# Kernel optimization log

Hardware: AMD Instinct MI355X
Metric: run time of the kernel (lower is better)

## Reference

```python
import jax, jax.numpy as jnp
import numpy as np

B, T, I = 8, 8192, 128
E, J, K = 16, 128, 1024


def setup_inputs() -> dict:
    key = jax.random.key(0)
    k1, k2, k3 = jax.random.split(key, 3)
    X = jax.random.normal(k1, (B, T, I), dtype=jnp.float32)
    ind = jax.random.randint(k2, (B, E, K), 0, T, dtype=jnp.int64)
    # matches torch.rand(E, I, J): uniform [0, 1)
    W = jax.random.uniform(k3, (E, I, J), dtype=jnp.float32)
    return {"X": X, "ind": ind, "W": W}


def reference(X, ind, W):
    # Dense per-expert matmul over ALL tokens: Y[b,e,t,j] = sum_i X[b,t,i] W[e,i,j]
    # (torch expand is a broadcast view; einsum broadcasts directly)
    Y = jnp.einsum('bti,eij->betj', X, W)  # [B, E, T, J]
    # Gather selected tokens per (batch, expert) along the token axis
    Yg = jnp.take_along_axis(Y, ind[..., None], axis=2)  # [B, E, K, J]
    return Yg
```

## Files before the change

### kernel.cpp

```cpp
#include <hip/hip_runtime.h>

#define B_ 8
#define T_ 8192
#define I_ 128
#define E_ 16
#define J_ 128
#define K_ 1024
#define ROWS 128

typedef unsigned short u16;
typedef unsigned int   u32;
typedef __attribute__((ext_vector_type(8))) short s8v;
typedef __attribute__((ext_vector_type(4))) float f4v;

__device__ __forceinline__ u16 f2bf(float f) {
    union { float f; u32 u; } v; v.f = f;
    const u32 u = v.u;
    return (u16)((u + 0x7fffu + ((u >> 16) & 1u)) >> 16);
}

__global__ __launch_bounds__(512, 4)
void gather_mfma(const float* __restrict__ X, const int* __restrict__ ind,
                 const float* __restrict__ W, float* __restrict__ Y) {
    __shared__ u16 WsT[I_ * J_];
    __shared__ u16 Xs[ROWS * I_];

    const int t    = threadIdx.x;
    const int wave = t >> 6;
    const int lane = t & 63;

    const int orig = blockIdx.x;
    const int bid  = (orig & 7) * 64 + (orig >> 3);
    const int kh = bid & 3;
    const int be = bid >> 2;
    const int e  = be & (E_ - 1);
    const int b  = be >> 4;
    const int k0 = kh * (2 * ROWS);

    const int ch   = lane & 31;
    const int rsub = lane >> 5;
    int idxA[8], idxB[8];
#pragma unroll
    for (int u = 0; u < 8; ++u) {
        const int rw = wave * 2 + rsub + 16 * u;
        idxA[u] = ind[(size_t)be * K_ + k0 + rw];
        idxB[u] = ind[(size_t)be * K_ + k0 + ROWS + rw];
    }

    {
        const float* We = W + (size_t)e * (I_ * J_);
        const int io = t & 15;
        const int j0 = (t >> 4) * 4;
        float4 w4[8];
#pragma unroll
        for (int u = 0; u < 8; ++u)
            w4[u] = *reinterpret_cast<const float4*>(We + (size_t)(io * 8 + u) * J_ + j0);
#pragma unroll
        for (int qq = 0; qq < 4; ++qq) {
            const int j = j0 + qq;
            s8v o;
#pragma unroll
            for (int u = 0; u < 8; ++u) {
                const float* wf = reinterpret_cast<const float*>(&w4[u]);
                o[u] = (short)f2bf(wf[qq]);
            }
            *reinterpret_cast<s8v*>((char*)WsT + ((j * 256 + io * 16) ^ ((j & 7) << 4))) = o;
        }
    }

    float4 v[8];
    auto load_rows = [&](const int* idxs) {
#pragma unroll
        for (int u = 0; u < 8; ++u)
            v[u] = reinterpret_cast<const float4*>(X + ((size_t)b * T_ + idxs[u]) * I_)[ch];
    };
    auto pack_write = [&]() {
#pragma unroll
        for (int u = 0; u < 8; ++u) {
            const int rw = wave * 2 + rsub + 16 * u;
            const float4 a = v[u];
            uint2 o;
            o.x = ((u32)f2bf(a.y) << 16) | f2bf(a.x);
            o.y = ((u32)f2bf(a.w) << 16) | f2bf(a.z);
            *reinterpret_cast<uint2*>((char*)Xs + rw * 256 + ((ch * 8) ^ ((rw & 7) << 4))) = o;
        }
    };

    load_rows(idxA);
    pack_write();
    __syncthreads();

    const int rq  = wave >> 1;
    const int jh  = wave & 1;
    const int g   = lane >> 4;
    const int l15 = lane & 15;
    const int sx  = (lane & 7) << 4;
    const char* xb = (const char*)Xs  + (size_t)(rq * 32 + l15) * 256;
    const char* wb = (const char*)WsT + (size_t)(jh * 64 + l15) * 256;

    auto compute_store = [&](int kbase) {
        s8v af[2][4];
#pragma unroll
        for (int s = 0; s < 4; ++s) {
            const int off = (s * 64 + g * 16) ^ sx;
            af[0][s] = *reinterpret_cast<const s8v*>(xb + off);
            af[1][s] = *reinterpret_cast<const s8v*>(xb + 16 * 256 + off);
        }
        float* Yb = Y + ((size_t)be * K_ + kbase) * J_;
#pragma unroll
        for (int n = 0; n < 4; ++n) {
            f4v acc0, acc1;
#pragma unroll
            for (int rr = 0; rr < 4; ++rr) { acc0[rr] = 0.f; acc1[rr] = 0.f; }
#pragma unroll
            for (int s = 0; s < 4; ++s) {
                const int off = (s * 64 + g * 16) ^ sx;
                const s8v bf = *reinterpret_cast<const s8v*>(wb + n * 16 * 256 + off);
                acc0 = __builtin_amdgcn_mfma_f32_16x16x32_bf16(af[0][s], bf, acc0, 0, 0, 0);
                acc1 = __builtin_amdgcn_mfma_f32_16x16x32_bf16(af[1][s], bf, acc1, 0, 0, 0);
            }
            const int col = jh * 64 + n * 16 + l15;
            const int row0 = rq * 32 + g * 4;
#pragma unroll
            for (int rr = 0; rr < 4; ++rr)
                Yb[(size_t)(row0 + rr) * J_ + col] = acc0[rr];
#pragma unroll
            for (int rr = 0; rr < 4; ++rr)
                Yb[(size_t)(row0 + 16 + rr) * J_ + col] = acc1[rr];
        }
    };

    load_rows(idxB);
    compute_store(k0);
    __syncthreads();
    pack_write();
    __syncthreads();
    compute_store(k0 + ROWS);
}

extern "C" void kernel_launch(void* const* d_in, const int* in_sizes, int n_in,
                              void* d_out, int out_size, void* d_ws, size_t ws_size,
                              hipStream_t stream) {
    (void)in_sizes; (void)n_in; (void)out_size; (void)d_ws; (void)ws_size;
    const float* X   = (const float*)d_in[0];
    const int*   ind = (const int*)d_in[1];
    const float* W   = (const float*)d_in[2];
    float*       Y   = (float*)d_out;

    const int grid = B_ * E_ * (K_ / (2 * ROWS));
    hipLaunchKernelGGL(gather_mfma, dim3(grid), dim3(512), 0, stream,
                       X, ind, W, Y);
}
```

Baseline: 24.95 us.

## Double-buffer gathered X tiles in four 64-row stages

Each block's 256 rows are now split into four 64-row tiles using two LDS buffers (ping-pong), in place of two 128-row tiles sharing a single buffer. The pack-write of the next tile goes into the other buffer, so it can overlap with compute on the current one and one barrier per stage is dropped. Total LDS use is unchanged, but there are now more stages and barriers, and each wave does less MFMA work per stage, which lowers per-stage ILP.

```diff
diff --git a/kernel.cpp b/kernel.cpp
--- a/kernel.cpp
+++ b/kernel.cpp
@@ -6,7 +6,7 @@
 #define E_ 16
 #define J_ 128
 #define K_ 1024
-#define ROWS 128
+#define TR 64
 
 typedef unsigned short u16;
 typedef unsigned int   u32;
@@ -23,7 +23,8 @@
 void gather_mfma(const float* __restrict__ X, const int* __restrict__ ind,
                  const float* __restrict__ W, float* __restrict__ Y) {
     __shared__ u16 WsT[I_ * J_];
-    __shared__ u16 Xs[ROWS * I_];
+    __shared__ u16 XsA[TR * I_];
+    __shared__ u16 XsB[TR * I_];
 
     const int t    = threadIdx.x;
     const int wave = t >> 6;
@@ -35,17 +36,18 @@
     const int be = bid >> 2;
     const int e  = be & (E_ - 1);
     const int b  = be >> 4;
-    const int k0 = kh * (2 * ROWS);
+    const int k0 = kh * (4 * TR);
 
     const int ch   = lane & 31;
     const int rsub = lane >> 5;
-    int idxA[8], idxB[8];
+    int idx[4][4];
 #pragma unroll
-    for (int u = 0; u < 8; ++u) {
-        const int rw = wave * 2 + rsub + 16 * u;
-        idxA[u] = ind[(size_t)be * K_ + k0 + rw];
-        idxB[u] = ind[(size_t)be * K_ + k0 + ROWS + rw];
-    }
+    for (int tt = 0; tt < 4; ++tt)
+#pragma unroll
+        for (int u = 0; u < 4; ++u) {
+            const int rw = wave * 2 + rsub + 16 * u;
+            idx[tt][u] = ind[(size_t)be * K_ + k0 + tt * TR + rw];
+        }
 
     {
         const float* We = W + (size_t)e * (I_ * J_);
@@ -68,15 +70,15 @@
         }
     }
 
-    float4 v[8];
-    auto load_rows = [&](const int* idxs) {
+    float4 v[4];
+    auto load_rows = [&](const int (&ii)[4]) {
 #pragma unroll
-        for (int u = 0; u < 8; ++u)
-            v[u] = reinterpret_cast<const float4*>(X + ((size_t)b * T_ + idxs[u]) * I_)[ch];
+        for (int u = 0; u < 4; ++u)
+            v[u] = reinterpret_cast<const float4*>(X + ((size_t)b * T_ + ii[u]) * I_)[ch];
     };
-    auto pack_write = [&]() {
+    auto pack_write = [&](u16* Xs) {
 #pragma unroll
-        for (int u = 0; u < 8; ++u) {
+        for (int u = 0; u < 4; ++u) {
             const int rw = wave * 2 + rsub + 16 * u;
             const float4 a = v[u];
             uint2 o;
@@ -86,56 +88,60 @@
         }
     };
 
-    load_rows(idxA);
-    pack_write();
-    __syncthreads();
-
     const int rq  = wave >> 1;
     const int jh  = wave & 1;
     const int g   = lane >> 4;
     const int l15 = lane & 15;
     const int sx  = (lane & 7) << 4;
-    const char* xb = (const char*)Xs  + (size_t)(rq * 32 + l15) * 256;
     const char* wb = (const char*)WsT + (size_t)(jh * 64 + l15) * 256;
 
-    auto compute_store = [&](int kbase) {
-        s8v af[2][4];
+    auto compute_store = [&](const u16* Xs, int kbase) {
+        const char* xb = (const char*)Xs + (size_t)(rq * 16 + l15) * 256;
+        s8v af[4];
 #pragma unroll
         for (int s = 0; s < 4; ++s) {
             const int off = (s * 64 + g * 16) ^ sx;
-            af[0][s] = *reinterpret_cast<const s8v*>(xb + off);
-            af[1][s] = *reinterpret_cast<const s8v*>(xb + 16 * 256 + off);
+            af[s] = *reinterpret_cast<const s8v*>(xb + off);
         }
         float* Yb = Y + ((size_t)be * K_ + kbase) * J_;
 #pragma unroll
         for (int n = 0; n < 4; ++n) {
-            f4v acc0, acc1;
+            f4v acc;
 #pragma unroll
-            for (int rr = 0; rr < 4; ++rr) { acc0[rr] = 0.f; acc1[rr] = 0.f; }
+            for (int rr = 0; rr < 4; ++rr) acc[rr] = 0.f;
 #pragma unroll
             for (int s = 0; s < 4; ++s) {
                 const int off = (s * 64 + g * 16) ^ sx;
                 const s8v bf = *reinterpret_cast<const s8v*>(wb + n * 16 * 256 + off);
-                acc0 = __builtin_amdgcn_mfma_f32_16x16x32_bf16(af[0][s], bf, acc0, 0, 0, 0);
-                acc1 = __builtin_amdgcn_mfma_f32_16x16x32_bf16(af[1][s], bf, acc1, 0, 0, 0);
+                acc = __builtin_amdgcn_mfma_f32_16x16x32_bf16(af[s], bf, acc, 0, 0, 0);
             }
             const int col = jh * 64 + n * 16 + l15;
-            const int row0 = rq * 32 + g * 4;
+            const int row0 = rq * 16 + g * 4;
 #pragma unroll
             for (int rr = 0; rr < 4; ++rr)
-                Yb[(size_t)(row0 + rr) * J_ + col] = acc0[rr];
-#pragma unroll
-            for (int rr = 0; rr < 4; ++rr)
-                Yb[(size_t)(row0 + 16 + rr) * J_ + col] = acc1[rr];
+                Yb[(size_t)(row0 + rr) * J_ + col] = acc[rr];
         }
     };
 
-    load_rows(idxB);
-    compute_store(k0);
+    load_rows(idx[0]); pack_write(XsA);
     __syncthreads();
-    pack_write();
+
+    load_rows(idx[1]);
+    compute_store(XsA, k0);
+    pack_write(XsB);
     __syncthreads();
-    compute_store(k0 + ROWS);
+
+    load_rows(idx[2]);
+    compute_store(XsB, k0 + TR);
+    pack_write(XsA);
+    __syncthreads();
+
+    load_rows(idx[3]);
+    compute_store(XsA, k0 + 2 * TR);
+    pack_write(XsB);
+    __syncthreads();
+
+    compute_store(XsB, k0 + 3 * TR);
 }
 
 extern "C" void kernel_launch(void* const* d_in, const int* in_sizes, int n_in,
@@ -147,7 +153,7 @@
     const float* W   = (const float*)d_in[2];
     float*       Y   = (float*)d_out;
 
-    const int grid = B_ * E_ * (K_ / (2 * ROWS));
+    const int grid = B_ * E_ * (K_ / (4 * TR));
     hipLaunchKernelGGL(gather_mfma, dim3(grid), dim3(512), 0, stream,
                        X, ind, W, Y);
 }
```

Measured after the change: 24.37 us (median of 2 runs). -2.3%, faster.
